# Kernel tuning notes

Measured on AMD Instinct MI355X. Metric: run time of the kernel, lower is better.

The kernel has to match this reference:

```python
import jax, jax.numpy as jnp
import numpy as np

NUM_FREQS = 10  # positional-encoding frequency bands


def embed_fn(x, num_freqs=NUM_FREQS):
    # NeRF-style positional encoding of a [N, d] input -> [N, d*2*num_freqs]
    freqs = (2.0 ** jnp.arange(num_freqs)).astype(x.dtype)        # [F]
    xb = x[:, None, :] * freqs[None, :, None]                      # [N, F, d]
    enc = jnp.concatenate([jnp.sin(xb), jnp.cos(xb)], axis=-1)     # [N, F, 2d]
    return enc.reshape(x.shape[0], -1)                             # [N, 2*F*d]


def setup_inputs() -> dict:
    key = jax.random.key(0)
    k1, k2, k3, k4 = jax.random.split(key, 4)
    N, C, F = 262144, 256, NUM_FREQS
    D = 6 * 2 * F  # 120
    X = jax.random.normal(k1, (N, 6), dtype=jnp.float32)
    W = jax.random.normal(k2, (3 * C, D), dtype=jnp.float32) * 0.02  # linear_mappings
    weights = jax.random.uniform(k3, (3, N), dtype=jnp.float32)       # [k, N]
    cluster_ids = jax.random.randint(k4, (N, 3), 0, C)                # [N, k]
    return {"X": X, "W": W, "weights": weights, "cluster_ids": cluster_ids}


def reference(X, W, weights, cluster_ids):
    # mask: rows whose first 3 coords are all exactly -1 produce zero output
    mask = jnp.all(X[:, :3] == -1.0, axis=-1)                      # [N]
    enc = embed_fn(X)                                               # [N, D]
    # dense linear over ALL clusters: [N, D] @ [D, 3C] -> [N, C, 3]
    out_all = (enc @ W.T).reshape(enc.shape[0], -1, 3)
    # gather the k selected cluster outputs per token: [N, k, 3]
    sel = jnp.take_along_axis(out_all, cluster_ids[:, :, None], axis=1)
    # weighted sum over the k clusters (weights is [k, N])
    rgb = jnp.einsum('kn,nkc->nc', weights, sel)                    # [N, 3]
    # scatter into masked output: masked rows stay zero
    return jnp.where(mask[:, None], 0.0, rgb)
```

## Files before the change

kernel.cpp:

```cpp
#include <hip/hip_runtime.h>
#include <hip/hip_fp16.h>
#include <stdint.h>

#define FREQS 10
#define DDIM 120

typedef _Float16 half2v __attribute__((ext_vector_type(2)));

static __device__ __forceinline__ uint32_t pk(float lo, float hi) {
    half2v h = {(_Float16)lo, (_Float16)hi};
    return *(uint32_t*)&h;
}

static __device__ __forceinline__ float fdot2f(uint32_t a, uint32_t b, float c) {
#if __has_builtin(__builtin_amdgcn_fdot2)
    return __builtin_amdgcn_fdot2(*(half2v*)&a, *(half2v*)&b, c, false);
#else
    half2v av = *(half2v*)&a, bv = *(half2v*)&b;
    return fmaf((float)av.x, (float)bv.x, fmaf((float)av.y, (float)bv.y, c));
#endif
}

template <int CK, int RS>
__global__ __launch_bounds__(256) void convert_w(
    const float* __restrict__ W, uint4* __restrict__ Wp, int nclusters)
{
    int idx = blockIdx.x * blockDim.x + threadIdx.x;
    if (idx >= nclusters * CK) return;
    int c = idx / CK, ch = idx % CK;
    int wrow = ch / RS, cc = ch % RS;
    uint4 d = make_uint4(0u, 0u, 0u, 0u);
    if (cc < 15) {
        const float* src = W + ((size_t)(3 * c + wrow) * DDIM + cc * 8);
        float4 a = *(const float4*)(src);
        float4 b = *(const float4*)(src + 4);
        d.x = pk(a.x, a.y); d.y = pk(a.z, a.w);
        d.z = pk(b.x, b.y); d.w = pk(b.z, b.w);
    }
    Wp[idx] = d;
}

template <int CK, int RS>
__global__ __launch_bounds__(256, 4) void clnet_quad(
    const float* __restrict__ X,
    const uint4* __restrict__ Wp,
    const float* __restrict__ weights,
    const int*   __restrict__ ids,
    float*       __restrict__ out,
    int N)
{
    __shared__ uint32_t elds[64 * 68];

    const int tid = threadIdx.x;
    const int q = tid >> 2, l = tid & 3;
    const int n = blockIdx.x * 64 + q;
    const bool valid = (n < N);

    float x[6];
    bool mask = false;
    int cid[3] = {0, 0, 0};
    float wk[3] = {0.f, 0.f, 0.f};
    const unsigned eb = q * 68;

    if (valid) {
        const float2* xp = (const float2*)(X + (size_t)n * 6);
        float2 a0 = xp[0], a1 = xp[1], a2 = xp[2];
        x[0] = a0.x; x[1] = a0.y; x[2] = a1.x; x[3] = a1.y; x[4] = a2.x; x[5] = a2.y;
        mask = (x[0] == -1.0f) && (x[1] == -1.0f) && (x[2] == -1.0f);
#pragma unroll
        for (int k = 0; k < 3; ++k) {
            cid[k] = ids[(size_t)n * 3 + k];
            wk[k]  = weights[(size_t)k * N + n];
        }

#pragma unroll
        for (int fi = 0; fi < 3; ++fi) {
            int f = l + 4 * fi;
            if (f < FREQS) {
                float scale = (float)(1 << f);
                float s_[6], c_[6];
#pragma unroll
                for (int j = 0; j < 6; ++j) {
                    float v = x[j] * scale;
                    s_[j] = __sinf(v); c_[j] = __cosf(v);
                }
                unsigned o = eb + f * 6;
                *(uint2*)&elds[o + 0] = make_uint2(pk(s_[0], s_[1]), pk(s_[2], s_[3]));
                *(uint2*)&elds[o + 2] = make_uint2(pk(s_[4], s_[5]), pk(c_[0], c_[1]));
                *(uint2*)&elds[o + 4] = make_uint2(pk(c_[2], c_[3]), pk(c_[4], c_[5]));
            }
        }
        if (l == 3) {
            *(uint4*)&elds[eb + 60] = make_uint4(0u, 0u, 0u, 0u);
        }
    }

    __syncthreads();

    if (!valid) return;

    uint4 E[4];
#pragma unroll
    for (int j = 0; j < 4; ++j)
        E[j] = *(const uint4*)&elds[eb + (4 * j + l) * 4];

    float rgb[3] = {0.f, 0.f, 0.f};

#pragma unroll
    for (int k = 0; k < 3; ++k) {
        const uint4* base = Wp + (size_t)cid[k] * CK;
        float acc[3] = {0.f, 0.f, 0.f};
#pragma unroll
        for (int r = 0; r < 3; ++r) {
#pragma unroll
            for (int i = 0; i < 4; ++i) {
                if (RS == 16 || i < 3 || l < 3) {
                    uint4 wv = base[r * RS + 4 * i + l];
                    acc[r] = fdot2f(E[i].x, wv.x, acc[r]);
                    acc[r] = fdot2f(E[i].y, wv.y, acc[r]);
                    acc[r] = fdot2f(E[i].z, wv.z, acc[r]);
                    acc[r] = fdot2f(E[i].w, wv.w, acc[r]);
                }
            }
        }
        rgb[0] = fmaf(wk[k], acc[0], rgb[0]);
        rgb[1] = fmaf(wk[k], acc[1], rgb[1]);
        rgb[2] = fmaf(wk[k], acc[2], rgb[2]);
    }

#pragma unroll
    for (int r = 0; r < 3; ++r) {
        rgb[r] += __shfl_xor(rgb[r], 1);
        rgb[r] += __shfl_xor(rgb[r], 2);
    }

    if (l < 3) {
        float v = (l == 0) ? rgb[0] : (l == 1) ? rgb[1] : rgb[2];
        if (mask) v = 0.f;
        out[(size_t)n * 3 + l] = v;
    }
}

__global__ __launch_bounds__(256) void clnet_kernel_f32(
    const float* __restrict__ X, const float* __restrict__ W,
    const float* __restrict__ weights, const int* __restrict__ ids,
    float* __restrict__ out, int N)
{
    int n = blockIdx.x * blockDim.x + threadIdx.x;
    if (n >= N) return;
    const float2* xp = (const float2*)(X + (size_t)n * 6);
    float2 a0 = xp[0], a1 = xp[1], a2 = xp[2];
    float x[6] = {a0.x, a0.y, a1.x, a1.y, a2.x, a2.y};
    bool mask = (x[0] == -1.0f) && (x[1] == -1.0f) && (x[2] == -1.0f);

    float E[DDIM];
#pragma unroll
    for (int f = 0; f < FREQS; ++f) {
        float scale = (float)(1 << f);
#pragma unroll
        for (int j = 0; j < 6; ++j) {
            float v = x[j] * scale;
            E[f * 12 + j] = __sinf(v); E[f * 12 + 6 + j] = __cosf(v);
        }
    }
    float rgb[3] = {0.f, 0.f, 0.f};
#pragma unroll
    for (int k = 0; k < 3; ++k) {
        int cc = ids[(size_t)n * 3 + k];
        float wkk = weights[(size_t)k * N + n];
        const float4* wp = (const float4*)(W + (size_t)cc * (3 * DDIM));
        float acc[3] = {0.f, 0.f, 0.f};
#pragma unroll
        for (int ch = 0; ch < 90; ++ch) {
            float4 v = wp[ch];
            const int r = ch / 30, dbase = (ch % 30) * 4;
            acc[r] = fmaf(E[dbase + 0], v.x, acc[r]);
            acc[r] = fmaf(E[dbase + 1], v.y, acc[r]);
            acc[r] = fmaf(E[dbase + 2], v.z, acc[r]);
            acc[r] = fmaf(E[dbase + 3], v.w, acc[r]);
        }
        rgb[0] = fmaf(wkk, acc[0], rgb[0]);
        rgb[1] = fmaf(wkk, acc[1], rgb[1]);
        rgb[2] = fmaf(wkk, acc[2], rgb[2]);
    }
    if (mask) { rgb[0] = 0.f; rgb[1] = 0.f; rgb[2] = 0.f; }
    out[(size_t)n * 3 + 0] = rgb[0];
    out[(size_t)n * 3 + 1] = rgb[1];
    out[(size_t)n * 3 + 2] = rgb[2];
}

extern "C" void kernel_launch(void* const* d_in, const int* in_sizes, int n_in,
                              void* d_out, int out_size, void* d_ws, size_t ws_size,
                              hipStream_t stream)
{
    const float* X       = (const float*)d_in[0];
    const float* W       = (const float*)d_in[1];
    const float* weights = (const float*)d_in[2];
    const int*   ids     = (const int*)d_in[3];
    float*       out     = (float*)d_out;

    const int N = in_sizes[0] / 6;
    const int C = in_sizes[1] / (3 * DDIM);

    const size_t need48 = (size_t)C * 48 * 16;
    const size_t need45 = (size_t)C * 45 * 16;

    const int blk = 256;
    const int gridMain = (N + 63) / 64;

    if (ws_size >= need48) {
        uint4* Wp = (uint4*)d_ws;
        int nchunk = C * 48;
        convert_w<48, 16><<<(nchunk + blk - 1) / blk, blk, 0, stream>>>(W, Wp, C);
        clnet_quad<48, 16><<<gridMain, blk, 0, stream>>>(X, Wp, weights, ids, out, N);
    } else if (ws_size >= need45) {
        uint4* Wp = (uint4*)d_ws;
        int nchunk = C * 45;
        convert_w<45, 15><<<(nchunk + blk - 1) / blk, blk, 0, stream>>>(W, Wp, C);
        clnet_quad<45, 15><<<gridMain, blk, 0, stream>>>(X, Wp, weights, ids, out, N);
    } else {
        clnet_kernel_f32<<<(N + blk - 1) / blk, blk, 0, stream>>>(
            X, W, weights, ids, out, N);
    }
}
```

Before: 90.53 us.

## Sort token-cluster pairs by cluster and accumulate per-pair outputs with atomics

Replaces the per-token quad kernel with a counting-sort pipeline: histogram cluster ids, scan, and scatter (token,k,cluster) entries so that threads in a wave read the same cluster's fp16 weights. The main kernel handles one pair per thread, computes the encoding with double-angle recurrences instead of repeated sin/cos, and accumulates into the output with float atomics. This targets scattered weight loads and transcendental cost, but adds several extra launches, an entries buffer, output zeroing, atomic traffic, and some accuracy loss from the recurrence.

Result: slower. 239.3 us (+164.3%).

```diff
diff --git a/kernel.cpp b/kernel.cpp
--- a/kernel.cpp
+++ b/kernel.cpp
@@ -21,124 +21,161 @@
 #endif
 }
 
-template <int CK, int RS>
-__global__ __launch_bounds__(256) void convert_w(
-    const float* __restrict__ W, uint4* __restrict__ Wp, int nclusters)
-{
-    int idx = blockIdx.x * blockDim.x + threadIdx.x;
-    if (idx >= nclusters * CK) return;
-    int c = idx / CK, ch = idx % CK;
-    int wrow = ch / RS, cc = ch % RS;
-    uint4 d = make_uint4(0u, 0u, 0u, 0u);
-    if (cc < 15) {
-        const float* src = W + ((size_t)(3 * c + wrow) * DDIM + cc * 8);
-        float4 a = *(const float4*)(src);
-        float4 b = *(const float4*)(src + 4);
-        d.x = pk(a.x, a.y); d.y = pk(a.z, a.w);
-        d.z = pk(b.x, b.y); d.w = pk(b.z, b.w);
-    }
-    Wp[idx] = d;
-}
-
-template <int CK, int RS>
-__global__ __launch_bounds__(256, 4) void clnet_quad(
+static __device__ __forceinline__ void atomAddF(float* p, float v) {
+#if defined(__HIP_DEVICE_COMPILE__) && defined(__AMDGCN__)
+    unsafeAtomicAdd(p, v);
+#else
+    atomicAdd(p, v);
+#endif
+}
+
+__global__ __launch_bounds__(256) void convert_w_f16(
+    const float4* __restrict__ W4, uint2* __restrict__ Wh4, int n4)
+{
+    int i = blockIdx.x * blockDim.x + threadIdx.x;
+    if (i < n4) {
+        float4 v = W4[i];
+        Wh4[i] = make_uint2(pk(v.x, v.y), pk(v.z, v.w));
+    }
+}
+
+__global__ __launch_bounds__(256) void zero_misc(
+    float* __restrict__ out, int n_out, uint32_t* __restrict__ hist, int C)
+{
+    int i = blockIdx.x * blockDim.x + threadIdx.x;
+    if (i < n_out) out[i] = 0.f;
+    if (i < C)     hist[i] = 0u;
+}
+
+__global__ __launch_bounds__(256) void count_k(
+    const int* __restrict__ ids, uint32_t* __restrict__ hist, int N)
+{
+    __shared__ uint32_t lh[256];
+    int t = threadIdx.x;
+    lh[t] = 0u;
+    __syncthreads();
+    int n = blockIdx.x * 256 + t;
+    if (n < N) {
+        atomicAdd(&lh[ids[3 * n + 0]], 1u);
+        atomicAdd(&lh[ids[3 * n + 1]], 1u);
+        atomicAdd(&lh[ids[3 * n + 2]], 1u);
+    }
+    __syncthreads();
+    uint32_t v = lh[t];
+    if (v) atomicAdd(&hist[t], v);
+}
+
+__global__ __launch_bounds__(256) void scan_k(
+    const uint32_t* __restrict__ hist, uint32_t* __restrict__ cursor, int C)
+{
+    __shared__ uint32_t s[256];
+    int t = threadIdx.x;
+    uint32_t v = (t < C) ? hist[t] : 0u;
+    s[t] = v;
+    __syncthreads();
+    for (int off = 1; off < 256; off <<= 1) {
+        uint32_t add = (t >= off) ? s[t - off] : 0u;
+        __syncthreads();
+        s[t] += add;
+        __syncthreads();
+    }
+    if (t < C) cursor[t] = s[t] - v;
+}
+
+__global__ __launch_bounds__(256) void scatter_k(
+    const int* __restrict__ ids, uint32_t* __restrict__ cursor,
+    uint32_t* __restrict__ entries, int N)
+{
+    __shared__ uint32_t lh[256];
+    __shared__ uint32_t gbase[256];
+    int t = threadIdx.x;
+    lh[t] = 0u;
+    __syncthreads();
+    int n = blockIdx.x * 256 + t;
+    bool v = (n < N);
+    uint32_t c_[3], lr[3];
+    if (v) {
+#pragma unroll
+        for (int k = 0; k < 3; ++k) {
+            c_[k] = (uint32_t)ids[3 * n + k];
+            lr[k] = atomicAdd(&lh[c_[k]], 1u);
+        }
+    }
+    __syncthreads();
+    uint32_t cnt = lh[t];
+    if (cnt) gbase[t] = atomicAdd(&cursor[t], cnt);
+    __syncthreads();
+    if (v) {
+#pragma unroll
+        for (int k = 0; k < 3; ++k)
+            entries[gbase[c_[k]] + lr[k]] =
+                (uint32_t)n | ((uint32_t)k << 20) | (c_[k] << 22);
+    }
+}
+
+__global__ __launch_bounds__(256) void main_k(
     const float* __restrict__ X,
-    const uint4* __restrict__ Wp,
+    const uint16_t* __restrict__ Wh,
     const float* __restrict__ weights,
-    const int*   __restrict__ ids,
-    float*       __restrict__ out,
-    int N)
-{
-    __shared__ uint32_t elds[64 * 68];
-
-    const int tid = threadIdx.x;
-    const int q = tid >> 2, l = tid & 3;
-    const int n = blockIdx.x * 64 + q;
-    const bool valid = (n < N);
-
-    float x[6];
-    bool mask = false;
-    int cid[3] = {0, 0, 0};
-    float wk[3] = {0.f, 0.f, 0.f};
-    const unsigned eb = q * 68;
-
-    if (valid) {
-        const float2* xp = (const float2*)(X + (size_t)n * 6);
-        float2 a0 = xp[0], a1 = xp[1], a2 = xp[2];
-        x[0] = a0.x; x[1] = a0.y; x[2] = a1.x; x[3] = a1.y; x[4] = a2.x; x[5] = a2.y;
-        mask = (x[0] == -1.0f) && (x[1] == -1.0f) && (x[2] == -1.0f);
-#pragma unroll
-        for (int k = 0; k < 3; ++k) {
-            cid[k] = ids[(size_t)n * 3 + k];
-            wk[k]  = weights[(size_t)k * N + n];
-        }
-
-#pragma unroll
-        for (int fi = 0; fi < 3; ++fi) {
-            int f = l + 4 * fi;
-            if (f < FREQS) {
-                float scale = (float)(1 << f);
-                float s_[6], c_[6];
-#pragma unroll
-                for (int j = 0; j < 6; ++j) {
-                    float v = x[j] * scale;
-                    s_[j] = __sinf(v); c_[j] = __cosf(v);
-                }
-                unsigned o = eb + f * 6;
-                *(uint2*)&elds[o + 0] = make_uint2(pk(s_[0], s_[1]), pk(s_[2], s_[3]));
-                *(uint2*)&elds[o + 2] = make_uint2(pk(s_[4], s_[5]), pk(c_[0], c_[1]));
-                *(uint2*)&elds[o + 4] = make_uint2(pk(c_[2], c_[3]), pk(c_[4], c_[5]));
+    const uint32_t* __restrict__ entries,
+    float* __restrict__ out,
+    int N, int M)
+{
+    int g = blockIdx.x * 256 + threadIdx.x;
+    if (g >= M) return;
+    uint32_t e = entries[g];
+    int n = (int)(e & 0xFFFFFu);
+    int k = (int)((e >> 20) & 3u);
+    int c = (int)(e >> 22);
+
+    const float2* xp = (const float2*)(X + (size_t)n * 6);
+    float2 a0 = xp[0], a1 = xp[1], a2 = xp[2];
+    float x[6] = {a0.x, a0.y, a1.x, a1.y, a2.x, a2.y};
+    if (x[0] == -1.0f && x[1] == -1.0f && x[2] == -1.0f) return;
+
+    float wk = weights[(size_t)k * N + n];
+
+    float s_[6], c_[6];
+#pragma unroll
+    for (int j = 0; j < 6; ++j) { s_[j] = __sinf(x[j]); c_[j] = __cosf(x[j]); }
+
+    uint32_t E[60];
+#pragma unroll
+    for (int f = 0; f < FREQS; ++f) {
+        E[f * 6 + 0] = pk(s_[0], s_[1]);
+        E[f * 6 + 1] = pk(s_[2], s_[3]);
+        E[f * 6 + 2] = pk(s_[4], s_[5]);
+        E[f * 6 + 3] = pk(c_[0], c_[1]);
+        E[f * 6 + 4] = pk(c_[2], c_[3]);
+        E[f * 6 + 5] = pk(c_[4], c_[5]);
+        if (f < FREQS - 1) {
+#pragma unroll
+            for (int j = 0; j < 6; ++j) {
+                float ts = s_[j] + s_[j];
+                float sn = ts * c_[j];
+                float cn = fmaf(-ts, s_[j], 1.0f);
+                s_[j] = sn; c_[j] = cn;
             }
         }
-        if (l == 3) {
-            *(uint4*)&elds[eb + 60] = make_uint4(0u, 0u, 0u, 0u);
-        }
-    }
-
-    __syncthreads();
-
-    if (!valid) return;
-
-    uint4 E[4];
-#pragma unroll
-    for (int j = 0; j < 4; ++j)
-        E[j] = *(const uint4*)&elds[eb + (4 * j + l) * 4];
-
-    float rgb[3] = {0.f, 0.f, 0.f};
-
-#pragma unroll
-    for (int k = 0; k < 3; ++k) {
-        const uint4* base = Wp + (size_t)cid[k] * CK;
-        float acc[3] = {0.f, 0.f, 0.f};
-#pragma unroll
-        for (int r = 0; r < 3; ++r) {
-#pragma unroll
-            for (int i = 0; i < 4; ++i) {
-                if (RS == 16 || i < 3 || l < 3) {
-                    uint4 wv = base[r * RS + 4 * i + l];
-                    acc[r] = fdot2f(E[i].x, wv.x, acc[r]);
-                    acc[r] = fdot2f(E[i].y, wv.y, acc[r]);
-                    acc[r] = fdot2f(E[i].z, wv.z, acc[r]);
-                    acc[r] = fdot2f(E[i].w, wv.w, acc[r]);
-                }
-            }
-        }
-        rgb[0] = fmaf(wk[k], acc[0], rgb[0]);
-        rgb[1] = fmaf(wk[k], acc[1], rgb[1]);
-        rgb[2] = fmaf(wk[k], acc[2], rgb[2]);
-    }
-
-#pragma unroll
-    for (int r = 0; r < 3; ++r) {
-        rgb[r] += __shfl_xor(rgb[r], 1);
-        rgb[r] += __shfl_xor(rgb[r], 2);
-    }
-
-    if (l < 3) {
-        float v = (l == 0) ? rgb[0] : (l == 1) ? rgb[1] : rgb[2];
-        if (mask) v = 0.f;
-        out[(size_t)n * 3 + l] = v;
-    }
+    }
+
+    const uint4* wb = (const uint4*)(Wh + (size_t)c * (3 * DDIM));
+    float acc[3] = {0.f, 0.f, 0.f};
+#pragma unroll
+    for (int ch = 0; ch < 45; ++ch) {
+        const int r  = ch / 15;
+        const int cc = ch % 15;
+        uint4 wv = wb[ch];
+        acc[r] = fdot2f(E[cc * 4 + 0], wv.x, acc[r]);
+        acc[r] = fdot2f(E[cc * 4 + 1], wv.y, acc[r]);
+        acc[r] = fdot2f(E[cc * 4 + 2], wv.z, acc[r]);
+        acc[r] = fdot2f(E[cc * 4 + 3], wv.w, acc[r]);
+    }
+
+    float* op = out + (size_t)n * 3;
+    atomAddF(op + 0, wk * acc[0]);
+    atomAddF(op + 1, wk * acc[1]);
+    atomAddF(op + 2, wk * acc[2]);
 }
 
 __global__ __launch_bounds__(256) void clnet_kernel_f32(
@@ -201,23 +238,32 @@
 
     const int N = in_sizes[0] / 6;
     const int C = in_sizes[1] / (3 * DDIM);
-
-    const size_t need48 = (size_t)C * 48 * 16;
-    const size_t need45 = (size_t)C * 45 * 16;
+    const int M = 3 * N;
+
+    const size_t wh_bytes   = (size_t)C * 3 * DDIM * 2;
+    const size_t hist_off   = wh_bytes;
+    const size_t cursor_off = hist_off + (size_t)C * 4;
+    const size_t entry_off  = cursor_off + (size_t)C * 4;
+    const size_t need       = entry_off + (size_t)M * 4;
 
     const int blk = 256;
-    const int gridMain = (N + 63) / 64;
-
-    if (ws_size >= need48) {
-        uint4* Wp = (uint4*)d_ws;
-        int nchunk = C * 48;
-        convert_w<48, 16><<<(nchunk + blk - 1) / blk, blk, 0, stream>>>(W, Wp, C);
-        clnet_quad<48, 16><<<gridMain, blk, 0, stream>>>(X, Wp, weights, ids, out, N);
-    } else if (ws_size >= need45) {
-        uint4* Wp = (uint4*)d_ws;
-        int nchunk = C * 45;
-        convert_w<45, 15><<<(nchunk + blk - 1) / blk, blk, 0, stream>>>(W, Wp, C);
-        clnet_quad<45, 15><<<gridMain, blk, 0, stream>>>(X, Wp, weights, ids, out, N);
+
+    if (ws_size >= need && C <= 256 && N < (1 << 20)) {
+        char* ws = (char*)d_ws;
+        uint16_t* Wh      = (uint16_t*)(ws);
+        uint32_t* hist    = (uint32_t*)(ws + hist_off);
+        uint32_t* cursor  = (uint32_t*)(ws + cursor_off);
+        uint32_t* entries = (uint32_t*)(ws + entry_off);
+
+        int n4 = (C * 3 * DDIM) / 4;
+        convert_w_f16<<<(n4 + blk - 1) / blk, blk, 0, stream>>>(
+            (const float4*)W, (uint2*)Wh, n4);
+        zero_misc<<<(M + blk - 1) / blk, blk, 0, stream>>>(out, M, hist, C);
+        count_k<<<(N + blk - 1) / blk, blk, 0, stream>>>(ids, hist, N);
+        scan_k<<<1, blk, 0, stream>>>(hist, cursor, C);
+        scatter_k<<<(N + blk - 1) / blk, blk, 0, stream>>>(ids, cursor, entries, N);
+        main_k<<<(M + blk - 1) / blk, blk, 0, stream>>>(
+            X, Wh, weights, entries, out, N, M);
     } else {
         clnet_kernel_f32<<<(N + blk - 1) / blk, blk, 0, stream>>>(
             X, W, weights, ids, out, N);
```
